# Kernel optimization log

Hardware: AMD Instinct MI355X
Metric: run time of the kernel (lower is better)

## Reference

```python
import jax, jax.numpy as jnp
import numpy as np

N_NODES = 100_000
N_EDGES = 1_000_000
VOCAB = 10_000
HID = 75
OUT = 64
BN_EPS = 1e-5


def gcn_conv(x, edge_index, W, b, n):
    # PyG GCNConv: add self-loops, symmetric deg^{-1/2} normalization, then scatter-add.
    loop = jnp.arange(n, dtype=edge_index.dtype)
    src = jnp.concatenate([edge_index[0], loop])
    dst = jnp.concatenate([edge_index[1], loop])
    deg = jax.ops.segment_sum(jnp.ones_like(src, dtype=x.dtype), dst, num_segments=n)
    dinv = jnp.where(deg > 0, jax.lax.rsqrt(deg), 0.0)
    norm = dinv[src] * dinv[dst]              # [E+N]
    h = x @ W                                  # linear before propagate (PyG order)
    msg = h[src] * norm[:, None]               # gather + per-edge scale
    out = jax.ops.segment_sum(msg, dst, num_segments=n)
    return out + b


def batch_norm(x, gamma, beta):
    # BatchNorm1d over nodes, training mode (biased variance)
    mu = jnp.mean(x, axis=0)
    var = jnp.mean(jnp.square(x - mu), axis=0)
    return (x - mu) * jax.lax.rsqrt(var + BN_EPS) * gamma + beta


def setup_inputs() -> dict:
    key = jax.random.key(0)
    ks = jax.random.split(key, 8)
    x = jax.random.randint(ks[0], (N_NODES,), 0, VOCAB, dtype=jnp.int64)
    edge_index = jax.random.randint(ks[1], (2, N_EDGES), 0, N_NODES, dtype=jnp.int64)
    emb = jax.random.normal(ks[2], (VOCAB, HID), dtype=jnp.float32)
    scale = 1.0 / np.sqrt(HID)
    Ws = jax.random.normal(ks[3], (4, HID, HID), dtype=jnp.float32) * scale
    bs = jnp.zeros((4, HID), dtype=jnp.float32)
    gammas = jnp.ones((4, HID), dtype=jnp.float32)
    betas = jnp.zeros((4, HID), dtype=jnp.float32)
    W_mu = jax.random.normal(ks[4], (HID, OUT), dtype=jnp.float32) * scale
    b_mu = jnp.zeros((OUT,), dtype=jnp.float32)
    W_logstd = jax.random.normal(ks[5], (HID, OUT), dtype=jnp.float32) * scale
    b_logstd = jnp.zeros((OUT,), dtype=jnp.float32)
    return {"x": x, "edge_index": edge_index, "emb": emb, "Ws": Ws, "bs": bs,
            "gammas": gammas, "betas": betas, "W_mu": W_mu, "b_mu": b_mu,
            "W_logstd": W_logstd, "b_logstd": b_logstd}


def reference(x, edge_index, emb, Ws, bs, gammas, betas, W_mu, b_mu, W_logstd, b_logstd):
    h = emb[x]  # [N, 75] embedding lookup
    for i in range(4):
        h = jax.nn.relu(batch_norm(gcn_conv(h, edge_index, Ws[i], bs[i], N_NODES), gammas[i], betas[i]))
    mu = gcn_conv(h, edge_index, W_mu, b_mu, N_NODES)
    logstd = gcn_conv(h, edge_index, W_logstd, b_logstd, N_NODES)
    return (mu, logstd)
```

## Files before the change

kernel.cpp:

```cpp
#include <hip/hip_runtime.h>

#define NN 100000
#define NE 1000000
#define HID 75
#define SP 80
#define OUTF 64
#define BN_EPS 1e-5f
#define KP 104

#define SCAN_ELEMS 1024
#define SCAN_NBLK ((NN + SCAN_ELEMS - 1) / SCAN_ELEMS)

typedef short bf16x8 __attribute__((ext_vector_type(8)));
typedef float f32x4  __attribute__((ext_vector_type(4)));

__device__ __forceinline__ ushort f2bf(float f) {
    unsigned u = __float_as_uint(f);
    u += 0x7FFF + ((u >> 16) & 1);
    return (ushort)(u >> 16);
}
__device__ __forceinline__ float bf_lo(unsigned u) { return __uint_as_float(u << 16); }
__device__ __forceinline__ float bf_hi(unsigned u) { return __uint_as_float(u & 0xFFFF0000u); }

__global__ void hist_kernel(const int* __restrict__ dst, int* __restrict__ hist, int E) {
    int e = blockIdx.x * blockDim.x + threadIdx.x;
    if (e < E) atomicAdd(&hist[dst[e]], 1);
}

__global__ void dinv_kernel(const int* __restrict__ hist, float* __restrict__ dinv, int n) {
    int i = blockIdx.x * blockDim.x + threadIdx.x;
    if (i < n) dinv[i] = rsqrtf((float)hist[i] + 1.0f);
}

__global__ void scan_pass1(const int* __restrict__ hist, int* __restrict__ bsum) {
    __shared__ int sdata[256];
    int base = blockIdx.x * SCAN_ELEMS;
    int t = threadIdx.x;
    int s = 0;
    #pragma unroll
    for (int k = 0; k < 4; ++k) {
        int i = base + t * 4 + k;
        if (i < NN) s += hist[i];
    }
    sdata[t] = s;
    __syncthreads();
    for (int off = 128; off > 0; off >>= 1) {
        if (t < off) sdata[t] += sdata[t + off];
        __syncthreads();
    }
    if (t == 0) bsum[blockIdx.x] = sdata[0];
}

__global__ void scan_pass2(int* __restrict__ bsum, int* __restrict__ row_ptr, int nblk) {
    if (threadIdx.x == 0) {
        int acc = 0;
        for (int i = 0; i < nblk; ++i) { int v = bsum[i]; bsum[i] = acc; acc += v; }
        row_ptr[NN] = acc;
    }
}

__global__ void scan_pass3(const int* __restrict__ hist, const int* __restrict__ bsum,
                           int* __restrict__ row_ptr) {
    __shared__ int sdata[256];
    int base = blockIdx.x * SCAN_ELEMS;
    int t = threadIdx.x;
    int v[4];
    int s = 0;
    #pragma unroll
    for (int k = 0; k < 4; ++k) {
        int i = base + t * 4 + k;
        v[k] = (i < NN) ? hist[i] : 0;
        s += v[k];
    }
    sdata[t] = s;
    __syncthreads();
    for (int off = 1; off < 256; off <<= 1) {
        int x = (t >= off) ? sdata[t - off] : 0;
        __syncthreads();
        sdata[t] += x;
        __syncthreads();
    }
    int pre = bsum[blockIdx.x] + sdata[t] - s;
    #pragma unroll
    for (int k = 0; k < 4; ++k) {
        int i = base + t * 4 + k;
        if (i < NN) { row_ptr[i] = pre; pre += v[k]; }
    }
}

__global__ void csr_fill(const int* __restrict__ src, const int* __restrict__ dst,
                         const int* __restrict__ row_ptr, int* __restrict__ cnt,
                         int* __restrict__ col, int E) {
    int e = blockIdx.x * blockDim.x + threadIdx.x;
    if (e >= E) return;
    int d = dst[e];
    int slot = row_ptr[d] + atomicAdd(&cnt[d], 1);
    col[slot] = src[e];
}

__global__ void deg_hist_kernel(const int* __restrict__ hist, int* __restrict__ dh) {
    __shared__ int lh[64];
    if (threadIdx.x < 64) lh[threadIdx.x] = 0;
    __syncthreads();
    int i = blockIdx.x * 256 + threadIdx.x;
    if (i < NN) atomicAdd(&lh[min(hist[i], 63)], 1);
    __syncthreads();
    if (threadIdx.x < 64 && lh[threadIdx.x]) atomicAdd(&dh[threadIdx.x], lh[threadIdx.x]);
}

__global__ void deg_scan_kernel(const int* __restrict__ dh, int* __restrict__ doff) {
    if (threadIdx.x == 0) {
        int acc = 0;
        for (int d = 0; d < 64; ++d) { doff[d] = acc; acc += dh[d]; }
    }
}

__global__ void perm_fill_kernel(const int* __restrict__ hist, int* __restrict__ doff,
                                 int* __restrict__ perm) {
    __shared__ int lcnt[64];
    __shared__ int gbase[64];
    if (threadIdx.x < 64) lcnt[threadIdx.x] = 0;
    __syncthreads();
    int i = blockIdx.x * 256 + threadIdx.x;
    int d = 0, lrank = 0;
    bool act = (i < NN);
    if (act) { d = min(hist[i], 63); lrank = atomicAdd(&lcnt[d], 1); }
    __syncthreads();
    if (threadIdx.x < 64) {
        int c = lcnt[threadIdx.x];
        gbase[threadIdx.x] = c ? atomicAdd(&doff[threadIdx.x], c) : 0;
    }
    __syncthreads();
    if (act) perm[gbase[d] + lrank] = i;
}

__global__ void embed_kernel(const int* __restrict__ x, const float* __restrict__ emb,
                             float* __restrict__ h) {
    int t = blockIdx.x * blockDim.x + threadIdx.x;
    if (t >= NN * SP) return;
    int node = t / SP, f = t % SP;
    h[t] = (f < HID) ? emb[x[node] * HID + f] : 0.0f;
}

template<int J, bool BNRELU>
__global__ __launch_bounds__(256, 2)
void gemm_mfma(const float* __restrict__ h, const float* __restrict__ W,
               const float* __restrict__ ab, const float* __restrict__ dinv,
               ushort* __restrict__ outb) {
    constexpr int NT = (J + 15) / 16;
    constexpr int JP = NT * 16;
    constexpr int OS = JP;
    __shared__ ushort Wl[JP * KP];
    __shared__ ushort Hl[64 * KP];
    int tl = threadIdx.x;
    int rbase = blockIdx.x * 64;
    for (int idx = tl; idx < 96 * JP; idx += 256) {
        int k = idx / JP, n = idx % JP;
        float v = (k < HID && n < J) ? W[k * J + n] : 0.0f;
        Wl[n * KP + k] = f2bf(v);
    }
    for (int idx = tl; idx < 64 * 20; idx += 256) {
        int r = idx / 20, c = idx % 20;
        int row = rbase + r; if (row >= NN) row = NN - 1;
        float4 v = reinterpret_cast<const float4*>(h + (size_t)row * SP)[c];
        if (BNRELU) {
            float4 a4 = reinterpret_cast<const float4*>(ab)[c];
            float4 c4 = reinterpret_cast<const float4*>(ab + SP)[c];
            v.x = fmaxf(fmaf(v.x, a4.x, c4.x), 0.f);
            v.y = fmaxf(fmaf(v.y, a4.y, c4.y), 0.f);
            v.z = fmaxf(fmaf(v.z, a4.z, c4.z), 0.f);
            v.w = fmaxf(fmaf(v.w, a4.w, c4.w), 0.f);
        }
        ushort4 u;
        u.x = f2bf(v.x); u.y = f2bf(v.y); u.z = f2bf(v.z); u.w = f2bf(v.w);
        *reinterpret_cast<ushort4*>(&Hl[r * KP + c * 4]) = u;
    }
    for (int idx = tl; idx < 64 * 16; idx += 256) {
        int r = idx / 16, k = 80 + (idx % 16);
        Hl[r * KP + k] = 0;
    }
    __syncthreads();
    int w = tl >> 6;
    int l = tl & 63;
    int cq = l & 15;
    int q  = l >> 4;
    f32x4 acc[NT] = {};
    #pragma unroll
    for (int ks = 0; ks < 3; ++ks) {
        int k0 = ks * 32 + q * 8;
        bf16x8 a = *reinterpret_cast<const bf16x8*>(&Hl[(w * 16 + cq) * KP + k0]);
        #pragma unroll
        for (int t = 0; t < NT; ++t) {
            bf16x8 b = *reinterpret_cast<const bf16x8*>(&Wl[(t * 16 + cq) * KP + k0]);
            acc[t] = __builtin_amdgcn_mfma_f32_16x16x32_bf16(a, b, acc[t], 0, 0, 0);
        }
    }
    int r0 = rbase + w * 16 + q * 4;
    #pragma unroll
    for (int r = 0; r < 4; ++r) {
        int grow = r0 + r;
        if (grow < NN) {
            float d = dinv[grow];
            ushort* orow = outb + (size_t)grow * OS;
            #pragma unroll
            for (int t = 0; t < NT; ++t)
                orow[t * 16 + cq] = f2bf(acc[t][r] * d);
        }
    }
}

__global__ __launch_bounds__(256, 2)
void gemm_mfma_dual(const float* __restrict__ h, const float* __restrict__ Wmu,
                    const float* __restrict__ Wls, const float* __restrict__ ab,
                    const float* __restrict__ dinv, ushort* __restrict__ outb) {
    constexpr int NT = 8;
    constexpr int JP = 128;
    __shared__ ushort Wl[JP * KP];
    __shared__ ushort Hl[64 * KP];
    int tl = threadIdx.x;
    int rbase = blockIdx.x * 64;
    for (int idx = tl; idx < 96 * JP; idx += 256) {
        int k = idx / JP, n = idx % JP;
        float v = 0.f;
        if (k < HID) v = (n < 64) ? Wmu[k * 64 + n] : Wls[k * 64 + (n - 64)];
        Wl[n * KP + k] = f2bf(v);
    }
    for (int idx = tl; idx < 64 * 20; idx += 256) {
        int r = idx / 20, c = idx % 20;
        int row = rbase + r; if (row >= NN) row = NN - 1;
        float4 v = reinterpret_cast<const float4*>(h + (size_t)row * SP)[c];
        float4 a4 = reinterpret_cast<const float4*>(ab)[c];
        float4 c4 = reinterpret_cast<const float4*>(ab + SP)[c];
        v.x = fmaxf(fmaf(v.x, a4.x, c4.x), 0.f);
        v.y = fmaxf(fmaf(v.y, a4.y, c4.y), 0.f);
        v.z = fmaxf(fmaf(v.z, a4.z, c4.z), 0.f);
        v.w = fmaxf(fmaf(v.w, a4.w, c4.w), 0.f);
        ushort4 u;
        u.x = f2bf(v.x); u.y = f2bf(v.y); u.z = f2bf(v.z); u.w = f2bf(v.w);
        *reinterpret_cast<ushort4*>(&Hl[r * KP + c * 4]) = u;
    }
    for (int idx = tl; idx < 64 * 16; idx += 256) {
        int r = idx / 16, k = 80 + (idx % 16);
        Hl[r * KP + k] = 0;
    }
    __syncthreads();
    int w = tl >> 6;
    int l = tl & 63;
    int cq = l & 15;
    int q  = l >> 4;
    f32x4 acc[NT] = {};
    #pragma unroll
    for (int ks = 0; ks < 3; ++ks) {
        int k0 = ks * 32 + q * 8;
        bf16x8 a = *reinterpret_cast<const bf16x8*>(&Hl[(w * 16 + cq) * KP + k0]);
        #pragma unroll
        for (int t = 0; t < NT; ++t) {
            bf16x8 b = *reinterpret_cast<const bf16x8*>(&Wl[(t * 16 + cq) * KP + k0]);
            acc[t] = __builtin_amdgcn_mfma_f32_16x16x32_bf16(a, b, acc[t], 0, 0, 0);
        }
    }
    int r0 = rbase + w * 16 + q * 4;
    #pragma unroll
    for (int r = 0; r < 4; ++r) {
        int grow = r0 + r;
        if (grow < NN) {
            float d = dinv[grow];
            ushort* orow = outb + (size_t)grow * 128;
            #pragma unroll
            for (int t = 0; t < NT; ++t)
                orow[t * 16 + cq] = f2bf(acc[t][r] * d);
        }
    }
}

#define ACCUM(W) \
    a0 += bf_lo(W.x); a1 += bf_hi(W.x); a2 += bf_lo(W.y); a3 += bf_hi(W.y);

__global__ void gather75(const int* __restrict__ row_ptr, const int* __restrict__ col,
                         const int* __restrict__ perm,
                         const uint2* __restrict__ hWb, const float* __restrict__ dinv,
                         float* __restrict__ agg) {
    int t = blockIdx.x * 256 + threadIdx.x;
    if (t >= NN * 20) return;
    int n = perm[t / 20];
    int c = t % 20;
    int beg = row_ptr[n], end = row_ptr[n + 1];
    uint2 v = hWb[(size_t)n * 20 + c];
    float a0 = bf_lo(v.x), a1 = bf_hi(v.x), a2 = bf_lo(v.y), a3 = bf_hi(v.y);
    int e = beg;
    for (; e + 3 < end; e += 4) {
        int s0 = col[e], s1 = col[e + 1], s2 = col[e + 2], s3 = col[e + 3];
        uint2 w0 = hWb[(size_t)s0 * 20 + c];
        uint2 w1 = hWb[(size_t)s1 * 20 + c];
        uint2 w2 = hWb[(size_t)s2 * 20 + c];
        uint2 w3 = hWb[(size_t)s3 * 20 + c];
        ACCUM(w0) ACCUM(w1) ACCUM(w2) ACCUM(w3)
    }
    for (; e < end; ++e) {
        uint2 w0 = hWb[(size_t)col[e] * 20 + c];
        ACCUM(w0)
    }
    float d = dinv[n];
    reinterpret_cast<float4*>(agg)[(size_t)n * 20 + c] =
        make_float4(a0 * d, a1 * d, a2 * d, a3 * d);
}

__global__ void gather128(const int* __restrict__ row_ptr, const int* __restrict__ col,
                          const int* __restrict__ perm,
                          const uint2* __restrict__ hWb, const float* __restrict__ dinv,
                          const float* __restrict__ b_mu, const float* __restrict__ b_ls,
                          float* __restrict__ out_mu, float* __restrict__ out_ls) {
    int t = blockIdx.x * 256 + threadIdx.x;
    int n = perm[t >> 5];
    int c = t & 31;
    int beg = row_ptr[n], end = row_ptr[n + 1];
    uint2 v = hWb[(size_t)n * 32 + c];
    float a0 = bf_lo(v.x), a1 = bf_hi(v.x), a2 = bf_lo(v.y), a3 = bf_hi(v.y);
    int e = beg;
    for (; e + 3 < end; e += 4) {
        int s0 = col[e], s1 = col[e + 1], s2 = col[e + 2], s3 = col[e + 3];
        uint2 w0 = hWb[(size_t)s0 * 32 + c];
        uint2 w1 = hWb[(size_t)s1 * 32 + c];
        uint2 w2 = hWb[(size_t)s2 * 32 + c];
        uint2 w3 = hWb[(size_t)s3 * 32 + c];
        ACCUM(w0) ACCUM(w1) ACCUM(w2) ACCUM(w3)
    }
    for (; e < end; ++e) {
        uint2 w0 = hWb[(size_t)col[e] * 32 + c];
        ACCUM(w0)
    }
    float d = dinv[n];
    const float* bp = (c < 16) ? (b_mu + c * 4) : (b_ls + (c - 16) * 4);
    float* op = (c < 16) ? (out_mu + (size_t)n * 64 + c * 4)
                         : (out_ls + (size_t)n * 64 + (c - 16) * 4);
    float4 b = *reinterpret_cast<const float4*>(bp);
    *reinterpret_cast<float4*>(op) =
        make_float4(fmaf(a0, d, b.x), fmaf(a1, d, b.y), fmaf(a2, d, b.z), fmaf(a3, d, b.w));
}

__global__ void stats_kernel(const float* __restrict__ agg, float* __restrict__ stats) {
    __shared__ float ssum[SP], ssq[SP];
    if (threadIdx.x < SP) { ssum[threadIdx.x] = 0.f; ssq[threadIdx.x] = 0.f; }
    __syncthreads();
    int gtid = blockIdx.x * blockDim.x + threadIdx.x;
    int T = gridDim.x * blockDim.x;
    int c = gtid % 20;
    int r = gtid / 20;
    int rstep = T / 20;
    float4 s = make_float4(0.f, 0.f, 0.f, 0.f), q = make_float4(0.f, 0.f, 0.f, 0.f);
    for (; r < NN; r += rstep) {
        float4 v = reinterpret_cast<const float4*>(agg)[r * 20 + c];
        s.x += v.x; s.y += v.y; s.z += v.z; s.w += v.w;
        q.x += v.x * v.x; q.y += v.y * v.y; q.z += v.z * v.z; q.w += v.w * v.w;
    }
    atomicAdd(&ssum[c * 4 + 0], s.x); atomicAdd(&ssum[c * 4 + 1], s.y);
    atomicAdd(&ssum[c * 4 + 2], s.z); atomicAdd(&ssum[c * 4 + 3], s.w);
    atomicAdd(&ssq[c * 4 + 0], q.x); atomicAdd(&ssq[c * 4 + 1], q.y);
    atomicAdd(&ssq[c * 4 + 2], q.z); atomicAdd(&ssq[c * 4 + 3], q.w);
    __syncthreads();
    if (threadIdx.x < SP) {
        atomicAdd(&stats[threadIdx.x], ssum[threadIdx.x]);
        atomicAdd(&stats[SP + threadIdx.x], ssq[threadIdx.x]);
    }
}

__global__ void bn_finalize(const float* __restrict__ stats, const float* __restrict__ gamma,
                            const float* __restrict__ beta, float* __restrict__ ab) {
    int f = threadIdx.x;
    if (f >= SP) return;
    float a = 0.f, cc = 0.f;
    if (f < HID) {
        float mu = stats[f] * (1.0f / NN);
        float var = stats[SP + f] * (1.0f / NN) - mu * mu;
        a = gamma[f] * rsqrtf(var + BN_EPS);
        cc = beta[f] - mu * a;
    }
    ab[f] = a;
    ab[SP + f] = cc;
}

extern "C" void kernel_launch(void* const* d_in, const int* in_sizes, int n_in,
                              void* d_out, int out_size, void* d_ws, size_t ws_size,
                              hipStream_t stream) {
    const int*   x      = (const int*)d_in[0];
    const int*   ei     = (const int*)d_in[1];
    const float* emb    = (const float*)d_in[2];
    const float* Ws     = (const float*)d_in[3];
    const float* gammas = (const float*)d_in[5];
    const float* betas  = (const float*)d_in[6];
    const float* W_mu   = (const float*)d_in[7];
    const float* b_mu   = (const float*)d_in[8];
    const float* W_ls   = (const float*)d_in[9];
    const float* b_ls   = (const float*)d_in[10];
    float* out = (float*)d_out;

    const int E = in_sizes[1] / 2;
    const int* src = ei;
    const int* dst = ei + E;

    char* ws = (char*)d_ws;
    float*  dinv    = (float*) (ws + 0);
    float*  stats   = (float*) (ws + 400000);
    float*  ab      = (float*) (ws + 400640);
    int*    hist    = (int*)   (ws + 401408);
    int*    row_ptr = (int*)   (ws + 801408);
    int*    cnt     = (int*)   (ws + 1201536);
    int*    bsum    = (int*)   (ws + 1601536);
    int*    col     = (int*)   (ws + 1602048);
    float*  hA      = (float*) (ws + 5602048);
    ushort* hBb     = (ushort*)(ws + 37602048);
    int*    perm    = (int*)   (ws + 63202048);
    int*    dh      = (int*)   (ws + 63602048);
    int*    doff    = (int*)   (ws + 63602304);

    hipMemsetAsync(hist, 0, NN * sizeof(int), stream);
    hist_kernel<<<(E + 255) / 256, 256, 0, stream>>>(dst, hist, E);
    dinv_kernel<<<(NN + 255) / 256, 256, 0, stream>>>(hist, dinv, NN);
    scan_pass1<<<SCAN_NBLK, 256, 0, stream>>>(hist, bsum);
    scan_pass2<<<1, 64, 0, stream>>>(bsum, row_ptr, SCAN_NBLK);
    scan_pass3<<<SCAN_NBLK, 256, 0, stream>>>(hist, bsum, row_ptr);
    hipMemsetAsync(cnt, 0, NN * sizeof(int), stream);
    csr_fill<<<(E + 255) / 256, 256, 0, stream>>>(src, dst, row_ptr, cnt, col, E);

    hipMemsetAsync(dh, 0, 64 * sizeof(int), stream);
    deg_hist_kernel<<<(NN + 255) / 256, 256, 0, stream>>>(hist, dh);
    deg_scan_kernel<<<1, 64, 0, stream>>>(dh, doff);
    perm_fill_kernel<<<(NN + 255) / 256, 256, 0, stream>>>(hist, doff, perm);

    embed_kernel<<<(NN * SP + 255) / 256, 256, 0, stream>>>(x, emb, hA);

    for (int layer = 0; layer < 4; ++layer) {
        const float* W = Ws + (size_t)layer * HID * HID;
        if (layer == 0)
            gemm_mfma<HID, false><<<(NN + 63) / 64, 256, 0, stream>>>(hA, W, ab, dinv, hBb);
        else
            gemm_mfma<HID, true><<<(NN + 63) / 64, 256, 0, stream>>>(hA, W, ab, dinv, hBb);
        gather75<<<(NN * 20 + 255) / 256, 256, 0, stream>>>(row_ptr, col, perm,
                                                            (const uint2*)hBb, dinv, hA);
        hipMemsetAsync(stats, 0, 2 * SP * sizeof(float), stream);
        stats_kernel<<<640, 256, 0, stream>>>(hA, stats);
        bn_finalize<<<1, 128, 0, stream>>>(stats, gammas + layer * HID, betas + layer * HID, ab);
    }

    float* out2 = out + (size_t)NN * OUTF;
    gemm_mfma_dual<<<(NN + 63) / 64, 256, 0, stream>>>(hA, W_mu, W_ls, ab, dinv, hBb);
    gather128<<<(NN * 32) / 256, 256, 0, stream>>>(row_ptr, col, perm, (const uint2*)hBb,
                                                   dinv, b_mu, b_ls, out, out2);
}
```

Before: 631.1 us.

## Store activations in bf16, drop degree-sorted permutation, merge memsets

The intermediate node activations (embedding output and aggregated features) are now stored as bf16 instead of fp32, which halves the traffic in gather, stats and GEMM loads. The degree-bucket permutation (three kernels plus a memset) is removed, so the gathers process nodes in natural order. The separate memsets for hist, cnt and the per-layer stats are merged into one upfront memset, with a stats slot per layer. This trades load balance from degree sorting and some accuracy in the BN statistics for fewer launches and less memory traffic.

```diff
diff --git a/kernel.cpp b/kernel.cpp
--- a/kernel.cpp
+++ b/kernel.cpp
@@ -98,53 +98,17 @@
     col[slot] = src[e];
 }
 
-__global__ void deg_hist_kernel(const int* __restrict__ hist, int* __restrict__ dh) {
-    __shared__ int lh[64];
-    if (threadIdx.x < 64) lh[threadIdx.x] = 0;
-    __syncthreads();
-    int i = blockIdx.x * 256 + threadIdx.x;
-    if (i < NN) atomicAdd(&lh[min(hist[i], 63)], 1);
-    __syncthreads();
-    if (threadIdx.x < 64 && lh[threadIdx.x]) atomicAdd(&dh[threadIdx.x], lh[threadIdx.x]);
-}
-
-__global__ void deg_scan_kernel(const int* __restrict__ dh, int* __restrict__ doff) {
-    if (threadIdx.x == 0) {
-        int acc = 0;
-        for (int d = 0; d < 64; ++d) { doff[d] = acc; acc += dh[d]; }
-    }
-}
-
-__global__ void perm_fill_kernel(const int* __restrict__ hist, int* __restrict__ doff,
-                                 int* __restrict__ perm) {
-    __shared__ int lcnt[64];
-    __shared__ int gbase[64];
-    if (threadIdx.x < 64) lcnt[threadIdx.x] = 0;
-    __syncthreads();
-    int i = blockIdx.x * 256 + threadIdx.x;
-    int d = 0, lrank = 0;
-    bool act = (i < NN);
-    if (act) { d = min(hist[i], 63); lrank = atomicAdd(&lcnt[d], 1); }
-    __syncthreads();
-    if (threadIdx.x < 64) {
-        int c = lcnt[threadIdx.x];
-        gbase[threadIdx.x] = c ? atomicAdd(&doff[threadIdx.x], c) : 0;
-    }
-    __syncthreads();
-    if (act) perm[gbase[d] + lrank] = i;
-}
-
 __global__ void embed_kernel(const int* __restrict__ x, const float* __restrict__ emb,
-                             float* __restrict__ h) {
+                             ushort* __restrict__ h) {
     int t = blockIdx.x * blockDim.x + threadIdx.x;
     if (t >= NN * SP) return;
     int node = t / SP, f = t % SP;
-    h[t] = (f < HID) ? emb[x[node] * HID + f] : 0.0f;
+    h[t] = (f < HID) ? f2bf(emb[x[node] * HID + f]) : (ushort)0;
 }
 
 template<int J, bool BNRELU>
 __global__ __launch_bounds__(256, 2)
-void gemm_mfma(const float* __restrict__ h, const float* __restrict__ W,
+void gemm_mfma(const ushort* __restrict__ h, const float* __restrict__ W,
                const float* __restrict__ ab, const float* __restrict__ dinv,
                ushort* __restrict__ outb) {
     constexpr int NT = (J + 15) / 16;
@@ -162,17 +126,20 @@
     for (int idx = tl; idx < 64 * 20; idx += 256) {
         int r = idx / 20, c = idx % 20;
         int row = rbase + r; if (row >= NN) row = NN - 1;
-        float4 v = reinterpret_cast<const float4*>(h + (size_t)row * SP)[c];
+        uint2 raw = reinterpret_cast<const uint2*>(h + (size_t)row * SP)[c];
+        ushort4 u;
         if (BNRELU) {
+            float v0 = bf_lo(raw.x), v1 = bf_hi(raw.x), v2 = bf_lo(raw.y), v3 = bf_hi(raw.y);
             float4 a4 = reinterpret_cast<const float4*>(ab)[c];
             float4 c4 = reinterpret_cast<const float4*>(ab + SP)[c];
-            v.x = fmaxf(fmaf(v.x, a4.x, c4.x), 0.f);
-            v.y = fmaxf(fmaf(v.y, a4.y, c4.y), 0.f);
-            v.z = fmaxf(fmaf(v.z, a4.z, c4.z), 0.f);
-            v.w = fmaxf(fmaf(v.w, a4.w, c4.w), 0.f);
+            u.x = f2bf(fmaxf(fmaf(v0, a4.x, c4.x), 0.f));
+            u.y = f2bf(fmaxf(fmaf(v1, a4.y, c4.y), 0.f));
+            u.z = f2bf(fmaxf(fmaf(v2, a4.z, c4.z), 0.f));
+            u.w = f2bf(fmaxf(fmaf(v3, a4.w, c4.w), 0.f));
+        } else {
+            u.x = (ushort)(raw.x & 0xFFFF); u.y = (ushort)(raw.x >> 16);
+            u.z = (ushort)(raw.y & 0xFFFF); u.w = (ushort)(raw.y >> 16);
         }
-        ushort4 u;
-        u.x = f2bf(v.x); u.y = f2bf(v.y); u.z = f2bf(v.z); u.w = f2bf(v.w);
         *reinterpret_cast<ushort4*>(&Hl[r * KP + c * 4]) = u;
     }
     for (int idx = tl; idx < 64 * 16; idx += 256) {
@@ -210,7 +177,7 @@
 }
 
 __global__ __launch_bounds__(256, 2)
-void gemm_mfma_dual(const float* __restrict__ h, const float* __restrict__ Wmu,
+void gemm_mfma_dual(const ushort* __restrict__ h, const float* __restrict__ Wmu,
                     const float* __restrict__ Wls, const float* __restrict__ ab,
                     const float* __restrict__ dinv, ushort* __restrict__ outb) {
     constexpr int NT = 8;
@@ -228,15 +195,15 @@
     for (int idx = tl; idx < 64 * 20; idx += 256) {
         int r = idx / 20, c = idx % 20;
         int row = rbase + r; if (row >= NN) row = NN - 1;
-        float4 v = reinterpret_cast<const float4*>(h + (size_t)row * SP)[c];
+        uint2 raw = reinterpret_cast<const uint2*>(h + (size_t)row * SP)[c];
+        float v0 = bf_lo(raw.x), v1 = bf_hi(raw.x), v2 = bf_lo(raw.y), v3 = bf_hi(raw.y);
         float4 a4 = reinterpret_cast<const float4*>(ab)[c];
         float4 c4 = reinterpret_cast<const float4*>(ab + SP)[c];
-        v.x = fmaxf(fmaf(v.x, a4.x, c4.x), 0.f);
-        v.y = fmaxf(fmaf(v.y, a4.y, c4.y), 0.f);
-        v.z = fmaxf(fmaf(v.z, a4.z, c4.z), 0.f);
-        v.w = fmaxf(fmaf(v.w, a4.w, c4.w), 0.f);
         ushort4 u;
-        u.x = f2bf(v.x); u.y = f2bf(v.y); u.z = f2bf(v.z); u.w = f2bf(v.w);
+        u.x = f2bf(fmaxf(fmaf(v0, a4.x, c4.x), 0.f));
+        u.y = f2bf(fmaxf(fmaf(v1, a4.y, c4.y), 0.f));
+        u.z = f2bf(fmaxf(fmaf(v2, a4.z, c4.z), 0.f));
+        u.w = f2bf(fmaxf(fmaf(v3, a4.w, c4.w), 0.f));
         *reinterpret_cast<ushort4*>(&Hl[r * KP + c * 4]) = u;
     }
     for (int idx = tl; idx < 64 * 16; idx += 256) {
@@ -277,13 +244,11 @@
     a0 += bf_lo(W.x); a1 += bf_hi(W.x); a2 += bf_lo(W.y); a3 += bf_hi(W.y);
 
 __global__ void gather75(const int* __restrict__ row_ptr, const int* __restrict__ col,
-                         const int* __restrict__ perm,
                          const uint2* __restrict__ hWb, const float* __restrict__ dinv,
-                         float* __restrict__ agg) {
+                         ushort* __restrict__ agg) {
     int t = blockIdx.x * 256 + threadIdx.x;
     if (t >= NN * 20) return;
-    int n = perm[t / 20];
-    int c = t % 20;
+    int n = t / 20, c = t % 20;
     int beg = row_ptr[n], end = row_ptr[n + 1];
     uint2 v = hWb[(size_t)n * 20 + c];
     float a0 = bf_lo(v.x), a1 = bf_hi(v.x), a2 = bf_lo(v.y), a3 = bf_hi(v.y);
@@ -301,17 +266,17 @@
         ACCUM(w0)
     }
     float d = dinv[n];
-    reinterpret_cast<float4*>(agg)[(size_t)n * 20 + c] =
-        make_float4(a0 * d, a1 * d, a2 * d, a3 * d);
+    ushort4 o;
+    o.x = f2bf(a0 * d); o.y = f2bf(a1 * d); o.z = f2bf(a2 * d); o.w = f2bf(a3 * d);
+    reinterpret_cast<ushort4*>(agg)[(size_t)n * 20 + c] = o;
 }
 
 __global__ void gather128(const int* __restrict__ row_ptr, const int* __restrict__ col,
-                          const int* __restrict__ perm,
                           const uint2* __restrict__ hWb, const float* __restrict__ dinv,
                           const float* __restrict__ b_mu, const float* __restrict__ b_ls,
                           float* __restrict__ out_mu, float* __restrict__ out_ls) {
     int t = blockIdx.x * 256 + threadIdx.x;
-    int n = perm[t >> 5];
+    int n = t >> 5;
     int c = t & 31;
     int beg = row_ptr[n], end = row_ptr[n + 1];
     uint2 v = hWb[(size_t)n * 32 + c];
@@ -338,29 +303,34 @@
         make_float4(fmaf(a0, d, b.x), fmaf(a1, d, b.y), fmaf(a2, d, b.z), fmaf(a3, d, b.w));
 }
 
-__global__ void stats_kernel(const float* __restrict__ agg, float* __restrict__ stats) {
+__global__ void stats_kernel(const ushort* __restrict__ agg, float* __restrict__ stats) {
     __shared__ float ssum[SP], ssq[SP];
-    if (threadIdx.x < SP) { ssum[threadIdx.x] = 0.f; ssq[threadIdx.x] = 0.f; }
-    __syncthreads();
-    int gtid = blockIdx.x * blockDim.x + threadIdx.x;
+    int tl = threadIdx.x;
+    if (tl < SP) { ssum[tl] = 0.f; ssq[tl] = 0.f; }
+    __syncthreads();
+    int gtid = blockIdx.x * blockDim.x + tl;
     int T = gridDim.x * blockDim.x;
     int c = gtid % 20;
     int r = gtid / 20;
     int rstep = T / 20;
-    float4 s = make_float4(0.f, 0.f, 0.f, 0.f), q = make_float4(0.f, 0.f, 0.f, 0.f);
+    float s0 = 0.f, s1 = 0.f, s2 = 0.f, s3 = 0.f;
+    float q0 = 0.f, q1 = 0.f, q2 = 0.f, q3 = 0.f;
+    const uint2* a2 = reinterpret_cast<const uint2*>(agg);
     for (; r < NN; r += rstep) {
-        float4 v = reinterpret_cast<const float4*>(agg)[r * 20 + c];
-        s.x += v.x; s.y += v.y; s.z += v.z; s.w += v.w;
-        q.x += v.x * v.x; q.y += v.y * v.y; q.z += v.z * v.z; q.w += v.w * v.w;
-    }
-    atomicAdd(&ssum[c * 4 + 0], s.x); atomicAdd(&ssum[c * 4 + 1], s.y);
-    atomicAdd(&ssum[c * 4 + 2], s.z); atomicAdd(&ssum[c * 4 + 3], s.w);
-    atomicAdd(&ssq[c * 4 + 0], q.x); atomicAdd(&ssq[c * 4 + 1], q.y);
-    atomicAdd(&ssq[c * 4 + 2], q.z); atomicAdd(&ssq[c * 4 + 3], q.w);
-    __syncthreads();
-    if (threadIdx.x < SP) {
-        atomicAdd(&stats[threadIdx.x], ssum[threadIdx.x]);
-        atomicAdd(&stats[SP + threadIdx.x], ssq[threadIdx.x]);
+        uint2 v = a2[r * 20 + c];
+        float v0 = bf_lo(v.x), v1 = bf_hi(v.x), v2 = bf_lo(v.y), v3 = bf_hi(v.y);
+        s0 += v0; s1 += v1; s2 += v2; s3 += v3;
+        q0 += v0 * v0; q1 += v1 * v1; q2 += v2 * v2; q3 += v3 * v3;
+    }
+    int fb = c * 4;
+    atomicAdd(&ssum[fb + 0], s0); atomicAdd(&ssq[fb + 0], q0);
+    atomicAdd(&ssum[fb + 1], s1); atomicAdd(&ssq[fb + 1], q1);
+    atomicAdd(&ssum[fb + 2], s2); atomicAdd(&ssq[fb + 2], q2);
+    atomicAdd(&ssum[fb + 3], s3); atomicAdd(&ssq[fb + 3], q3);
+    __syncthreads();
+    if (tl < SP) {
+        atomicAdd(&stats[tl], ssum[tl]);
+        atomicAdd(&stats[SP + tl], ssq[tl]);
     }
 }
 
@@ -399,51 +369,43 @@
     const int* dst = ei + E;
 
     char* ws = (char*)d_ws;
-    float*  dinv    = (float*) (ws + 0);
-    float*  stats   = (float*) (ws + 400000);
-    float*  ab      = (float*) (ws + 400640);
-    int*    hist    = (int*)   (ws + 401408);
-    int*    row_ptr = (int*)   (ws + 801408);
-    int*    cnt     = (int*)   (ws + 1201536);
-    int*    bsum    = (int*)   (ws + 1601536);
-    int*    col     = (int*)   (ws + 1602048);
-    float*  hA      = (float*) (ws + 5602048);
-    ushort* hBb     = (ushort*)(ws + 37602048);
-    int*    perm    = (int*)   (ws + 63202048);
-    int*    dh      = (int*)   (ws + 63602048);
-    int*    doff    = (int*)   (ws + 63602304);
-
-    hipMemsetAsync(hist, 0, NN * sizeof(int), stream);
+    int*    hist    = (int*)   (ws + 0);
+    int*    cnt     = (int*)   (ws + 400000);
+    float*  stats4  = (float*) (ws + 800000);
+    float*  dinv    = (float*) (ws + 803072);
+    float*  ab      = (float*) (ws + 1203072);
+    int*    bsum    = (int*)   (ws + 1203712);
+    int*    row_ptr = (int*)   (ws + 1204224);
+    int*    col     = (int*)   (ws + 1604352);
+    ushort* hA      = (ushort*)(ws + 5604352);
+    ushort* hBb     = (ushort*)(ws + 21604352);
+
+    hipMemsetAsync(ws, 0, 803072, stream);
+
     hist_kernel<<<(E + 255) / 256, 256, 0, stream>>>(dst, hist, E);
     dinv_kernel<<<(NN + 255) / 256, 256, 0, stream>>>(hist, dinv, NN);
     scan_pass1<<<SCAN_NBLK, 256, 0, stream>>>(hist, bsum);
     scan_pass2<<<1, 64, 0, stream>>>(bsum, row_ptr, SCAN_NBLK);
     scan_pass3<<<SCAN_NBLK, 256, 0, stream>>>(hist, bsum, row_ptr);
-    hipMemsetAsync(cnt, 0, NN * sizeof(int), stream);
     csr_fill<<<(E + 255) / 256, 256, 0, stream>>>(src, dst, row_ptr, cnt, col, E);
-
-    hipMemsetAsync(dh, 0, 64 * sizeof(int), stream);
-    deg_hist_kernel<<<(NN + 255) / 256, 256, 0, stream>>>(hist, dh);
-    deg_scan_kernel<<<1, 64, 0, stream>>>(dh, doff);
-    perm_fill_kernel<<<(NN + 255) / 256, 256, 0, stream>>>(hist, doff, perm);
 
     embed_kernel<<<(NN * SP + 255) / 256, 256, 0, stream>>>(x, emb, hA);
 
     for (int layer = 0; layer < 4; ++layer) {
         const float* W = Ws + (size_t)layer * HID * HID;
+        float* stats = stats4 + layer * 160;
         if (layer == 0)
             gemm_mfma<HID, false><<<(NN + 63) / 64, 256, 0, stream>>>(hA, W, ab, dinv, hBb);
         else
             gemm_mfma<HID, true><<<(NN + 63) / 64, 256, 0, stream>>>(hA, W, ab, dinv, hBb);
-        gather75<<<(NN * 20 + 255) / 256, 256, 0, stream>>>(row_ptr, col, perm,
+        gather75<<<(NN * 20 + 255) / 256, 256, 0, stream>>>(row_ptr, col,
                                                             (const uint2*)hBb, dinv, hA);
-        hipMemsetAsync(stats, 0, 2 * SP * sizeof(float), stream);
         stats_kernel<<<640, 256, 0, stream>>>(hA, stats);
         bn_finalize<<<1, 128, 0, stream>>>(stats, gammas + layer * HID, betas + layer * HID, ab);
     }
 
     float* out2 = out + (size_t)NN * OUTF;
     gemm_mfma_dual<<<(NN + 63) / 64, 256, 0, stream>>>(hA, W_mu, W_ls, ab, dinv, hBb);
-    gather128<<<(NN * 32) / 256, 256, 0, stream>>>(row_ptr, col, perm, (const uint2*)hBb,
+    gather128<<<(NN * 32) / 256, 256, 0, stream>>>(row_ptr, col, (const uint2*)hBb,
                                                    dinv, b_mu, b_ls, out, out2);
 }
```

Result: faster. 576.0 us (-8.7%).
